# Optimization experiments

Measured on AMD Instinct MI355X. Metric: run time of the kernel, lower is better.

The kernel has to match this reference:

```python
import jax, jax.numpy as jnp
import numpy as np

N_ATOMS = 200000
N_BONDS = 300000
E = 600000
D = 128
H = 128
EPS = 1e-5  # BatchNorm1d default eps


def setup_inputs() -> dict:
    key = jax.random.key(0)
    ks = jax.random.split(key, 8)
    x_atoms = jax.random.normal(ks[0], (N_ATOMS, D), jnp.float32)
    x_bonds = jax.random.normal(ks[1], (N_BONDS, D), jnp.float32)
    # atoms -> bonds edges: row0 src atom idx, row1 dst bond idx
    ei_ab = jnp.stack([
        jax.random.randint(ks[2], (E,), 0, N_ATOMS),
        jax.random.randint(ks[3], (E,), 0, N_BONDS),
    ]).astype(jnp.int64)
    # bonds -> atoms edges
    ei_ba = jnp.stack([
        jax.random.randint(ks[4], (E,), 0, N_BONDS),
        jax.random.randint(ks[5], (E,), 0, N_ATOMS),
    ]).astype(jnp.int64)
    xav = float(np.sqrt(6.0 / (D + H)))
    W = jax.random.uniform(ks[6], (H, D), jnp.float32, -xav, xav)   # shared lin_rel
    b = jnp.zeros((H,), jnp.float32)
    Wr = jax.random.uniform(ks[7], (H, D), jnp.float32, -xav, xav)  # res_connection
    br = jnp.zeros((H,), jnp.float32)
    return {
        "x_atoms": x_atoms, "x_bonds": x_bonds,
        "ei_ab": ei_ab, "ei_ba": ei_ba,
        "W": W, "b": b, "Wr": Wr, "br": br,
        "gamma_atoms": jnp.ones((H,), jnp.float32),
        "beta_atoms": jnp.zeros((H,), jnp.float32),
        "gamma_bonds": jnp.ones((H,), jnp.float32),
        "beta_bonds": jnp.zeros((H,), jnp.float32),
    }


def _bn(v, g, bt):
    # BatchNorm1d training-mode math: batch mean, biased variance
    m = v.mean(axis=0)
    var = v.var(axis=0)
    return (v - m) * jax.lax.rsqrt(var + EPS) * g + bt


def reference(x_atoms, x_bonds, ei_ab, ei_ba, W, b, Wr, br,
              gamma_atoms, beta_atoms, gamma_bonds, beta_bonds):
    # shared lin_rel applied to both node types
    h_atoms = x_atoms @ W.T + b   # [N_ATOMS, H]
    h_bonds = x_bonds @ W.T + b   # [N_BONDS, H]

    # message = lin(x_src)[src], aggregate = scatter-add at dst (source_to_target)
    agg_bonds = jax.ops.segment_sum(h_atoms[ei_ab[0]], ei_ab[1], num_segments=N_BONDS)
    agg_atoms = jax.ops.segment_sum(h_bonds[ei_ba[0]], ei_ba[1], num_segments=N_ATOMS)

    # residual: activation(res_connection(x))
    out_atoms = agg_atoms + jax.nn.relu(x_atoms @ Wr.T + br)
    out_bonds = agg_bonds + jax.nn.relu(x_bonds @ Wr.T + br)

    # dropout is identity in eval/deterministic reference
    out_atoms = _bn(out_atoms, gamma_atoms, beta_atoms)
    out_bonds = _bn(out_bonds, gamma_bonds, beta_bonds)
    return out_atoms, out_bonds
```

## Files before the change

kernel.cpp:

```cpp
#include <hip/hip_runtime.h>
#include <stdint.h>

#define NATOMS 200000
#define NBONDS 300000
#define NEDGE  600000
#define NSEG   (NATOMS + NBONDS)
#define DF     128
#define EPS    1e-5f
#define SCHUNK 2048
#define NSBLK  ((NSEG + SCHUNK - 1) / SCHUNK)
#define NGRP   (NSEG / 16)
#define NBUCK  32
#define NCHA   (NATOMS / 64)
#define NCHB   ((NBONDS + 63) / 64)
#define NCH    (NCHA + NCHB)

typedef __attribute__((ext_vector_type(8))) short bf16x8;
typedef __attribute__((ext_vector_type(4))) float f32x4;
typedef unsigned short u16;

__device__ __forceinline__ short f2b(float f) {
  union { float f; uint32_t u; } v; v.f = f;
  uint32_t r = v.u + 0x7fffu + ((v.u >> 16) & 1u);
  return (short)(r >> 16);
}
__device__ __forceinline__ float bf2f(u16 h) {
  union { uint32_t u; float f; } v; v.u = ((uint32_t)h) << 16; return v.f;
}
__device__ __forceinline__ bf16x8 pack8(float4 u, float4 v) {
  bf16x8 t;
  t[0] = f2b(u.x); t[1] = f2b(u.y); t[2] = f2b(u.z); t[3] = f2b(u.w);
  t[4] = f2b(v.x); t[5] = f2b(v.y); t[6] = f2b(v.z); t[7] = f2b(v.w);
  return t;
}

__global__ void k_prep(const float* __restrict__ W, const float* __restrict__ Wr,
                       u16* __restrict__ Wb, u16* __restrict__ Wrb) {
  int i = blockIdx.x * blockDim.x + threadIdx.x;
  if (i < DF * DF) {
    Wb[i]  = (u16)f2b(W[i]);
    Wrb[i] = (u16)f2b(Wr[i]);
  }
}

__global__ void k_setup(const float* __restrict__ xa, const float* __restrict__ xb,
                        u16* __restrict__ xaT, u16* __restrict__ xbT,
                        const int* __restrict__ ab, const int* __restrict__ ba,
                        int* __restrict__ cnt) {
  const int NA8 = NATOMS * DF / 8;
  const int NT8 = NSEG * DF / 8;
  int bid = blockIdx.x;
  if (bid < 4096) {
    int stride = 4096 * 256;
    for (int i = bid * 256 + threadIdx.x; i < NT8; i += stride) {
      const float* src; u16* dst; int j;
      if (i < NA8) { src = xa; dst = xaT; j = i; }
      else { src = xb; dst = xbT; j = i - NA8; }
      const float4 a = *(const float4*)(src + (size_t)j * 8);
      const float4 b = *(const float4*)(src + (size_t)j * 8 + 4);
      *(bf16x8*)(dst + (size_t)j * 8) = pack8(a, b);
    }
  } else {
    int stride = 512 * 256;
    for (int e = (bid - 4096) * 256 + threadIdx.x; e < 2 * NEDGE; e += stride) {
      int g;
      if (e < NEDGE) g = NATOMS + ab[NEDGE + e];
      else           g = ba[NEDGE + (e - NEDGE)];
      atomicAdd(cnt + g, 1);
    }
  }
}

__global__ void k_hist(const int* __restrict__ ab, const int* __restrict__ ba,
                       int* __restrict__ cnt) {
  int stride = gridDim.x * blockDim.x;
  for (int e = blockIdx.x * blockDim.x + threadIdx.x; e < 2 * NEDGE; e += stride) {
    int g;
    if (e < NEDGE) g = NATOMS + ab[NEDGE + e];
    else           g = ba[NEDGE + (e - NEDGE)];
    atomicAdd(cnt + g, 1);
  }
}

__global__ void k_scanA(const int* __restrict__ cnt, int* __restrict__ bsum) {
  __shared__ int wsm[4];
  int t = threadIdx.x;
  int base = blockIdx.x * SCHUNK + t * 8;
  int s = 0;
#pragma unroll
  for (int j = 0; j < 8; ++j) { int i = base + j; if (i < NSEG) s += cnt[i]; }
  for (int d = 1; d < 64; d <<= 1) s += __shfl_xor(s, d);
  if ((t & 63) == 0) wsm[t >> 6] = s;
  __syncthreads();
  if (t == 0) bsum[blockIdx.x] = wsm[0] + wsm[1] + wsm[2] + wsm[3];
}

__global__ void k_scanB(const int* __restrict__ bsum, int* __restrict__ bbase) {
  __shared__ int wsm[4];
  int t = threadIdx.x;
  int lane = t & 63;
  int v = (t < NSBLK) ? bsum[t] : 0;
  int s = v;
  for (int d = 1; d < 64; d <<= 1) { int n = __shfl_up(s, d); if (lane >= d) s += n; }
  if (lane == 63) wsm[t >> 6] = s;
  __syncthreads();
  int wbase = 0;
  for (int w = 0; w < (t >> 6); ++w) wbase += wsm[w];
  if (t < NSBLK) bbase[t] = wbase + s - v;
}

__global__ void k_scanC(const int* __restrict__ cnt, const int* __restrict__ bbase,
                        int* __restrict__ off, int* __restrict__ cursor) {
  __shared__ int wsm[4];
  int t = threadIdx.x;
  int lane = t & 63, wv = t >> 6;
  int base = blockIdx.x * SCHUNK + t * 8;
  int v[8]; int ts = 0;
#pragma unroll
  for (int j = 0; j < 8; ++j) { int i = base + j; v[j] = (i < NSEG) ? cnt[i] : 0; ts += v[j]; }
  int s = ts;
  for (int d = 1; d < 64; d <<= 1) { int n = __shfl_up(s, d); if (lane >= d) s += n; }
  if (lane == 63) wsm[wv] = s;
  __syncthreads();
  int wbase = bbase[blockIdx.x];
  for (int w = 0; w < wv; ++w) wbase += wsm[w];
  int run = wbase + s - ts;
#pragma unroll
  for (int j = 0; j < 8; ++j) {
    int i = base + j;
    if (i < NSEG) { off[i] = run; cursor[i] = run; }
    run += v[j];
  }
}

__global__ void k_fill(const int* __restrict__ ab, const int* __restrict__ ba,
                       int* __restrict__ cursor, int* __restrict__ sorted) {
  int stride = gridDim.x * blockDim.x;
  for (int e = blockIdx.x * blockDim.x + threadIdx.x; e < 2 * NEDGE; e += stride) {
    int g, src;
    if (e < NEDGE) { g = NATOMS + ab[NEDGE + e]; src = ab[e]; }
    else { int e2 = e - NEDGE; g = ba[NEDGE + e2]; src = ba[e2]; }
    int pos = atomicAdd(cursor + g, 1);
    sorted[pos] = src;
  }
}

__global__ void k_gather_b(const u16* __restrict__ xaT, const u16* __restrict__ xbT,
                           const int* __restrict__ sorted, const int* __restrict__ off,
                           const int* __restrict__ cnt, u16* __restrict__ aggT) {
  int lane = threadIdx.x & 63;
  int l16 = lane & 15, e4 = lane >> 4;
  int wid = (blockIdx.x * blockDim.x + threadIdx.x) >> 6;
  int nw = (gridDim.x * blockDim.x) >> 6;
  for (int g = wid; g < NSEG; g += nw) {
    int start = off[g], deg = cnt[g];
    const u16* src = (g < NATOMS) ? xbT : xaT;
    float acc[8];
#pragma unroll
    for (int j = 0; j < 8; ++j) acc[j] = 0.f;
    for (int k = e4; k < deg; k += 4) {
      int s = sorted[start + k];
      bf16x8 v = *(const bf16x8*)(src + (size_t)s * DF + l16 * 8);
#pragma unroll
      for (int j = 0; j < 8; ++j) acc[j] += bf2f((u16)v[j]);
    }
#pragma unroll
    for (int j = 0; j < 8; ++j) {
      acc[j] += __shfl_xor(acc[j], 16);
      acc[j] += __shfl_xor(acc[j], 32);
    }
    if (e4 == 0) {
      bf16x8 r;
#pragma unroll
      for (int j = 0; j < 8; ++j) r[j] = f2b(acc[j]);
      *(bf16x8*)(aggT + (size_t)g * DF + l16 * 8) = r;
    }
  }
}

__global__ void k_gather_f(const float* __restrict__ xa, const float* __restrict__ xb,
                           const int* __restrict__ sorted, const int* __restrict__ off,
                           const int* __restrict__ cnt, float* __restrict__ outf) {
  int l32 = threadIdx.x & 31;
  int hwid = (blockIdx.x * blockDim.x + threadIdx.x) >> 5;
  int nhw = (gridDim.x * blockDim.x) >> 5;
  for (int g = hwid; g < NSEG; g += nhw) {
    int start = off[g], deg = cnt[g];
    const float* src = (g < NATOMS) ? xb : xa;
    float a0 = 0.f, a1 = 0.f, a2 = 0.f, a3 = 0.f;
    int k = 0;
    for (; k + 1 < deg; k += 2) {
      int s0 = sorted[start + k], s1 = sorted[start + k + 1];
      float4 v0 = *(const float4*)(src + (size_t)s0 * DF + l32 * 4);
      float4 v1 = *(const float4*)(src + (size_t)s1 * DF + l32 * 4);
      a0 += v0.x + v1.x; a1 += v0.y + v1.y; a2 += v0.z + v1.z; a3 += v0.w + v1.w;
    }
    if (k < deg) {
      int s0 = sorted[start + k];
      float4 v0 = *(const float4*)(src + (size_t)s0 * DF + l32 * 4);
      a0 += v0.x; a1 += v0.y; a2 += v0.z; a3 += v0.w;
    }
    float4 r; r.x = a0; r.y = a1; r.z = a2; r.w = a3;
    *(float4*)(outf + (size_t)g * DF + l32 * 4) = r;
  }
}


#define LOADG(G, S) { \
  int sb_ = (G) << 4; \
  int typ_ = sb_ >= NATOMS; \
  const u16* ap_ = aggT + ((size_t)(sb_ + r16) << 7) + kq8; \
  const u16* xp_; \
  if (typ_) xp_ = xbT + ((size_t)(sb_ - NATOMS + r16) << 7) + kq8; \
  else      xp_ = xaT + ((size_t)(sb_ + r16) << 7) + kq8; \
  S##A0 = *(const bf16x8*)(ap_);      S##A1 = *(const bf16x8*)(ap_ + 32); \
  S##A2 = *(const bf16x8*)(ap_ + 64); S##A3 = *(const bf16x8*)(ap_ + 96); \
  S##X0 = *(const bf16x8*)(xp_);      S##X1 = *(const bf16x8*)(xp_ + 32); \
  S##X2 = *(const bf16x8*)(xp_ + 64); S##X3 = *(const bf16x8*)(xp_ + 96); \
  S##C0 = cnt[sb_ + kq4 + 0]; S##C1 = cnt[sb_ + kq4 + 1]; \
  S##C2 = cnt[sb_ + kq4 + 2]; S##C3 = cnt[sb_ + kq4 + 3]; \
}

#define COMPUTE(G, S) { \
  int sb_ = (G) << 4; \
  int typ_ = sb_ >= NATOMS; \
  f32x4 w0 = {0.f,0.f,0.f,0.f}, w1 = {0.f,0.f,0.f,0.f}; \
  f32x4 r0 = {0.f,0.f,0.f,0.f}, r1 = {0.f,0.f,0.f,0.f}; \
  w0 = __builtin_amdgcn_mfma_f32_16x16x32_bf16(S##A0, wf[0][0], w0, 0,0,0); \
  w1 = __builtin_amdgcn_mfma_f32_16x16x32_bf16(S##A0, wf[1][0], w1, 0,0,0); \
  r0 = __builtin_amdgcn_mfma_f32_16x16x32_bf16(S##X0, wrf[0][0], r0, 0,0,0); \
  r1 = __builtin_amdgcn_mfma_f32_16x16x32_bf16(S##X0, wrf[1][0], r1, 0,0,0); \
  w0 = __builtin_amdgcn_mfma_f32_16x16x32_bf16(S##A1, wf[0][1], w0, 0,0,0); \
  w1 = __builtin_amdgcn_mfma_f32_16x16x32_bf16(S##A1, wf[1][1], w1, 0,0,0); \
  r0 = __builtin_amdgcn_mfma_f32_16x16x32_bf16(S##X1, wrf[0][1], r0, 0,0,0); \
  r1 = __builtin_amdgcn_mfma_f32_16x16x32_bf16(S##X1, wrf[1][1], r1, 0,0,0); \
  w0 = __builtin_amdgcn_mfma_f32_16x16x32_bf16(S##A2, wf[0][2], w0, 0,0,0); \
  w1 = __builtin_amdgcn_mfma_f32_16x16x32_bf16(S##A2, wf[1][2], w1, 0,0,0); \
  r0 = __builtin_amdgcn_mfma_f32_16x16x32_bf16(S##X2, wrf[0][2], r0, 0,0,0); \
  r1 = __builtin_amdgcn_mfma_f32_16x16x32_bf16(S##X2, wrf[1][2], r1, 0,0,0); \
  w0 = __builtin_amdgcn_mfma_f32_16x16x32_bf16(S##A3, wf[0][3], w0, 0,0,0); \
  w1 = __builtin_amdgcn_mfma_f32_16x16x32_bf16(S##A3, wf[1][3], w1, 0,0,0); \
  r0 = __builtin_amdgcn_mfma_f32_16x16x32_bf16(S##X3, wrf[0][3], r0, 0,0,0); \
  r1 = __builtin_amdgcn_mfma_f32_16x16x32_bf16(S##X3, wrf[1][3], r1, 0,0,0); \
  const float cf0_ = (float)S##C0, cf1_ = (float)S##C1; \
  const float cf2_ = (float)S##C2, cf3_ = (float)S##C3; \
  u16* gp_ = gT + ((size_t)(sb_ + kq4) << 7) + t016 + r16; \
  float g0_, g1_, g2_, g3_, ss_, qq_; \
  g0_ = w0[0] + cf0_ * bvv0 + fmaxf(r0[0] + brr0, 0.f); \
  g1_ = w0[1] + cf1_ * bvv0 + fmaxf(r0[1] + brr0, 0.f); \
  g2_ = w0[2] + cf2_ * bvv0 + fmaxf(r0[2] + brr0, 0.f); \
  g3_ = w0[3] + cf3_ * bvv0 + fmaxf(r0[3] + brr0, 0.f); \
  gp_[0] = (u16)f2b(g0_); gp_[128] = (u16)f2b(g1_); \
  gp_[256] = (u16)f2b(g2_); gp_[384] = (u16)f2b(g3_); \
  ss_ = g0_ + g1_ + g2_ + g3_; \
  qq_ = g0_*g0_ + g1_*g1_ + g2_*g2_ + g3_*g3_; \
  if (typ_) { sB0 += ss_; qB0 += qq_; } else { sA0 += ss_; qA0 += qq_; } \
  g0_ = w1[0] + cf0_ * bvv1 + fmaxf(r1[0] + brr1, 0.f); \
  g1_ = w1[1] + cf1_ * bvv1 + fmaxf(r1[1] + brr1, 0.f); \
  g2_ = w1[2] + cf2_ * bvv1 + fmaxf(r1[2] + brr1, 0.f); \
  g3_ = w1[3] + cf3_ * bvv1 + fmaxf(r1[3] + brr1, 0.f); \
  gp_[16] = (u16)f2b(g0_); gp_[144] = (u16)f2b(g1_); \
  gp_[272] = (u16)f2b(g2_); gp_[400] = (u16)f2b(g3_); \
  ss_ = g0_ + g1_ + g2_ + g3_; \
  qq_ = g0_*g0_ + g1_*g1_ + g2_*g2_ + g3_*g3_; \
  if (typ_) { sB1 += ss_; qB1 += qq_; } else { sA1 += ss_; qA1 += qq_; } \
}

__global__ __launch_bounds__(256, 2) void k_gemm_p(
    const u16* __restrict__ xaT, const u16* __restrict__ xbT,
    const u16* __restrict__ aggT, u16* __restrict__ gT,
    const int* __restrict__ cnt,
    const u16* __restrict__ Wb, const u16* __restrict__ Wrb,
    const float* __restrict__ bb, const float* __restrict__ brb,
    float* __restrict__ stats) {
  int lane = threadIdx.x & 63;
  int wv = threadIdx.x >> 6;
  int r16 = lane & 15, kq = lane >> 4;
  int kq8 = kq * 8, kq4 = kq * 4;
  int t016 = wv * 32;

  bf16x8 wf[2][4], wrf[2][4];
#pragma unroll
  for (int ti = 0; ti < 2; ++ti) {
#pragma unroll
    for (int kk = 0; kk < 4; ++kk) {
      size_t o = (size_t)(t016 + ti * 16 + r16) * DF + kk * 32 + kq8;
      wf[ti][kk]  = *(const bf16x8*)(Wb + o);
      wrf[ti][kk] = *(const bf16x8*)(Wrb + o);
    }
  }
  float bvv0 = bb[t016 + r16],      brr0 = brb[t016 + r16];
  float bvv1 = bb[t016 + 16 + r16], brr1 = brb[t016 + 16 + r16];

  float sA0 = 0.f, sA1 = 0.f, qA0 = 0.f, qA1 = 0.f;
  float sB0 = 0.f, sB1 = 0.f, qB0 = 0.f, qB1 = 0.f;

  bf16x8 PA0, PA1, PA2, PA3, PX0, PX1, PX2, PX3;
  bf16x8 QA0, QA1, QA2, QA3, QX0, QX1, QX2, QX3;
  int PC0, PC1, PC2, PC3, QC0, QC1, QC2, QC3;

  int step = gridDim.x;
  int g = blockIdx.x;
  if (g < NGRP) { LOADG(g, P); }
  while (g < NGRP) {
    int gn = g + step;
    if (gn < NGRP) { LOADG(gn, Q); }
    COMPUTE(g, P);
    g = gn;
    if (g >= NGRP) break;
    gn = g + step;
    if (gn < NGRP) { LOADG(gn, P); }
    COMPUTE(g, Q);
    g = gn;
  }

  int bkt = blockIdx.x & (NBUCK - 1);
  float* p = stats + (size_t)bkt * 4 * DF;
  {
    float s0 = sA0, q0 = qA0, s1 = sB0, q1 = qB0;
    s0 += __shfl_xor(s0, 16); q0 += __shfl_xor(q0, 16);
    s1 += __shfl_xor(s1, 16); q1 += __shfl_xor(q1, 16);
    s0 += __shfl_xor(s0, 32); q0 += __shfl_xor(q0, 32);
    s1 += __shfl_xor(s1, 32); q1 += __shfl_xor(q1, 32);
    if (kq == 0) {
      int feat = t016 + r16;
      atomicAdd(p + 0 * DF + feat, s0);
      atomicAdd(p + 1 * DF + feat, q0);
      atomicAdd(p + 2 * DF + feat, s1);
      atomicAdd(p + 3 * DF + feat, q1);
    }
  }
  {
    float s0 = sA1, q0 = qA1, s1 = sB1, q1 = qB1;
    s0 += __shfl_xor(s0, 16); q0 += __shfl_xor(q0, 16);
    s1 += __shfl_xor(s1, 16); q1 += __shfl_xor(q1, 16);
    s0 += __shfl_xor(s0, 32); q0 += __shfl_xor(q0, 32);
    s1 += __shfl_xor(s1, 32); q1 += __shfl_xor(q1, 32);
    if (kq == 0) {
      int feat = t016 + 16 + r16;
      atomicAdd(p + 0 * DF + feat, s0);
      atomicAdd(p + 1 * DF + feat, q0);
      atomicAdd(p + 2 * DF + feat, s1);
      atomicAdd(p + 3 * DF + feat, q1);
    }
  }
}

__global__ __launch_bounds__(256, 2) void k_gemm0(
    const float* __restrict__ xa, const float* __restrict__ xb,
    float* __restrict__ outf, const int* __restrict__ cnt,
    const u16* __restrict__ Wb, const u16* __restrict__ Wrb,
    const float* __restrict__ bb, const float* __restrict__ brb,
    float* __restrict__ stats) {
  int lane = threadIdx.x & 63;
  int wv = threadIdx.x >> 6;
  int r16 = lane & 15, kq = lane >> 4;
  int t016 = wv * 32;

  bf16x8 wf[2][4], wrf[2][4];
#pragma unroll
  for (int ti = 0; ti < 2; ++ti) {
#pragma unroll
    for (int kk = 0; kk < 4; ++kk) {
      size_t o = (size_t)(t016 + ti * 16 + r16) * DF + kk * 32 + kq * 8;
      wf[ti][kk]  = *(const bf16x8*)(Wb + o);
      wrf[ti][kk] = *(const bf16x8*)(Wrb + o);
    }
  }
  float bvv[2] = { bb[t016 + r16], bb[t016 + 16 + r16] };
  float brr[2] = { brb[t016 + r16], brb[t016 + 16 + r16] };

  float sA[2] = {0.f, 0.f}, qA[2] = {0.f, 0.f};
  float sB[2] = {0.f, 0.f}, qB[2] = {0.f, 0.f};

  for (int c = blockIdx.x; c < NCH; c += gridDim.x) {
    int typ, nrows, goff, base;
    if (c < NCHA) { typ = 0; nrows = NATOMS; goff = 0; base = c * 64; }
    else { typ = 1; nrows = NBONDS; goff = NATOMS; base = (c - NCHA) * 64; }
    const float* xsrc = typ ? xb : xa;

#pragma unroll
    for (int rg = 0; rg < 4; ++rg) {
      int rowbase = base + rg * 16;
      if (rowbase < nrows) {
        int row = rowbase + r16;
        const float* ap = outf + (size_t)(goff + row) * DF + kq * 8;
        const float* xp = xsrc + (size_t)row * DF + kq * 8;
        bf16x8 fA[4], fX[4];
#pragma unroll
        for (int kk = 0; kk < 4; ++kk) {
          fA[kk] = pack8(*(const float4*)(ap + kk * 32), *(const float4*)(ap + kk * 32 + 4));
          fX[kk] = pack8(*(const float4*)(xp + kk * 32), *(const float4*)(xp + kk * 32 + 4));
        }
        __syncthreads();

        f32x4 accW[2], accR[2];
#pragma unroll
        for (int ti = 0; ti < 2; ++ti) {
#pragma unroll
          for (int r = 0; r < 4; ++r) { accW[ti][r] = 0.f; accR[ti][r] = 0.f; }
        }
#pragma unroll
        for (int kk = 0; kk < 4; ++kk) {
#pragma unroll
          for (int ti = 0; ti < 2; ++ti) {
            accW[ti] = __builtin_amdgcn_mfma_f32_16x16x32_bf16(fA[kk], wf[ti][kk], accW[ti], 0, 0, 0);
            accR[ti] = __builtin_amdgcn_mfma_f32_16x16x32_bf16(fX[kk], wrf[ti][kk], accR[ti], 0, 0, 0);
          }
        }
        float cf[4];
#pragma unroll
        for (int r = 0; r < 4; ++r)
          cf[r] = (float)cnt[goff + rowbase + kq * 4 + r];
#pragma unroll
        for (int ti = 0; ti < 2; ++ti) {
          int feat = t016 + ti * 16 + r16;
          float s = 0.f, q = 0.f;
#pragma unroll
          for (int r = 0; r < 4; ++r) {
            int grow = rowbase + kq * 4 + r;
            float gg = accW[ti][r] + cf[r] * bvv[ti] + fmaxf(accR[ti][r] + brr[ti], 0.f);
            outf[(size_t)(goff + grow) * DF + feat] = gg;
            s += gg; q += gg * gg;
          }
          if (typ == 0) { sA[ti] += s; qA[ti] += q; }
          else          { sB[ti] += s; qB[ti] += q; }
        }
      }
    }
  }

  int bkt = blockIdx.x & (NBUCK - 1);
  float* p = stats + (size_t)bkt * 4 * DF;
#pragma unroll
  for (int ti = 0; ti < 2; ++ti) {
    float s0 = sA[ti], q0 = qA[ti], s1 = sB[ti], q1 = qB[ti];
    s0 += __shfl_xor(s0, 16); q0 += __shfl_xor(q0, 16);
    s1 += __shfl_xor(s1, 16); q1 += __shfl_xor(q1, 16);
    s0 += __shfl_xor(s0, 32); q0 += __shfl_xor(q0, 32);
    s1 += __shfl_xor(s1, 32); q1 += __shfl_xor(q1, 32);
    if (kq == 0) {
      int feat = t016 + ti * 16 + r16;
      atomicAdd(p + 0 * DF + feat, s0);
      atomicAdd(p + 1 * DF + feat, q0);
      atomicAdd(p + 2 * DF + feat, s1);
      atomicAdd(p + 3 * DF + feat, q1);
    }
  }
}

__global__ void k_stats(const float* __restrict__ stats,
                        const float* __restrict__ ga, const float* __restrict__ bea,
                        const float* __restrict__ gb, const float* __restrict__ beb,
                        float* __restrict__ scale, float* __restrict__ shift) {
  int tid = threadIdx.x;
  if (tid < 2 * DF) {
    int t = tid >> 7, f = tid & (DF - 1);
    float S = 0.f, SS = 0.f;
    for (int bk = 0; bk < NBUCK; ++bk) {
      const float* p = stats + (size_t)bk * 4 * DF;
      S  += p[(2 * t) * DF + f];
      SS += p[(2 * t + 1) * DF + f];
    }
    float n = t ? (float)NBONDS : (float)NATOMS;
    float mean = S / n;
    float var = SS / n - mean * mean;
    float rstd = rsqrtf(var + EPS);
    float g = t ? gb[f] : ga[f];
    float be = t ? beb[f] : bea[f];
    scale[tid] = rstd * g;
    shift[tid] = be - mean * rstd * g;
  }
}

template<int TIER>
__global__ void k_norm(float* __restrict__ out, const u16* __restrict__ gT,
                       const float* __restrict__ scale, const float* __restrict__ shift) {
  if constexpr (TIER) {
    const size_t nv = (size_t)NSEG * DF / 8;
    size_t stride = (size_t)gridDim.x * blockDim.x;
    for (size_t i = (size_t)blockIdx.x * blockDim.x + threadIdx.x; i < nv; i += stride) {
      size_t e = i * 8;
      int t = e >= (size_t)NATOMS * DF;
      int f = (int)(e & (DF - 1));
      bf16x8 v = *(const bf16x8*)(gT + e);
      const float* sc = scale + t * DF + f;
      const float* sh = shift + t * DF + f;
      float4 o0, o1;
      o0.x = fmaf(bf2f((u16)v[0]), sc[0], sh[0]);
      o0.y = fmaf(bf2f((u16)v[1]), sc[1], sh[1]);
      o0.z = fmaf(bf2f((u16)v[2]), sc[2], sh[2]);
      o0.w = fmaf(bf2f((u16)v[3]), sc[3], sh[3]);
      o1.x = fmaf(bf2f((u16)v[4]), sc[4], sh[4]);
      o1.y = fmaf(bf2f((u16)v[5]), sc[5], sh[5]);
      o1.z = fmaf(bf2f((u16)v[6]), sc[6], sh[6]);
      o1.w = fmaf(bf2f((u16)v[7]), sc[7], sh[7]);
      *(float4*)(out + e) = o0;
      *(float4*)(out + e + 4) = o1;
    }
  } else {
    const size_t nv = (size_t)NSEG * DF / 4;
    size_t stride = (size_t)gridDim.x * blockDim.x;
    for (size_t i = (size_t)blockIdx.x * blockDim.x + threadIdx.x; i < nv; i += stride) {
      size_t e = i * 4;
      int t = e >= (size_t)NATOMS * DF;
      int f = (int)(e & (DF - 1));
      const float* sc = scale + t * DF + f;
      const float* sh = shift + t * DF + f;
      float4 v = ((float4*)out)[i];
      v.x = fmaf(v.x, sc[0], sh[0]);
      v.y = fmaf(v.y, sc[1], sh[1]);
      v.z = fmaf(v.z, sc[2], sh[2]);
      v.w = fmaf(v.w, sc[3], sh[3]);
      ((float4*)out)[i] = v;
    }
  }
}

extern "C" void kernel_launch(void* const* d_in, const int* in_sizes, int n_in,
                              void* d_out, int out_size, void* d_ws, size_t ws_size,
                              hipStream_t stream) {
  const float* xa  = (const float*)d_in[0];
  const float* xb  = (const float*)d_in[1];
  const int*   ab  = (const int*)d_in[2];
  const int*   ba  = (const int*)d_in[3];
  const float* W   = (const float*)d_in[4];
  const float* b   = (const float*)d_in[5];
  const float* Wr  = (const float*)d_in[6];
  const float* br  = (const float*)d_in[7];
  const float* ga  = (const float*)d_in[8];
  const float* bea = (const float*)d_in[9];
  const float* gb  = (const float*)d_in[10];
  const float* beb = (const float*)d_in[11];
  float* out = (float*)d_out;

  char* ws = (char*)d_ws;
  int*   cnt    = (int*)ws;
  int*   off    = (int*)(ws +  2000000);
  int*   cursor = (int*)(ws +  4000000);
  int*   sorted = (int*)(ws +  6000000);
  float* stats  = (float*)(ws + 10800000);
  int*   bsum   = (int*)(ws + 10865536);
  int*   bbase  = (int*)(ws + 10866560);
  u16*   Wbf    = (u16*)(ws + 10867584);
  u16*   Wrbf   = (u16*)(ws + 10900352);
  float* scale  = (float*)(ws + 10933120);
  float* shift  = (float*)(ws + 10934144);
  u16*   gT   = (u16*)(ws + 10935168);
  u16*   xaT  = (u16*)(ws + 138935168);
  u16*   xbT  = (u16*)(ws + 190135168);
  u16*   aggT = (u16*)(ws + 266935168);
  const bool xt = ws_size >= 394935168ull;

  hipMemsetAsync(cnt, 0, 2000000, stream);
  hipMemsetAsync(stats, 0, 65536, stream);

  k_prep<<<64, 256, 0, stream>>>(W, Wr, Wbf, Wrbf);
  if (xt) {
    k_setup<<<4608, 256, 0, stream>>>(xa, xb, xaT, xbT, ab, ba, cnt);
  } else {
    k_hist<<<2048, 256, 0, stream>>>(ab, ba, cnt);
  }
  k_scanA<<<NSBLK, 256, 0, stream>>>(cnt, bsum);
  k_scanB<<<1, 256, 0, stream>>>(bsum, bbase);
  k_scanC<<<NSBLK, 256, 0, stream>>>(cnt, bbase, off, cursor);
  k_fill<<<2048, 256, 0, stream>>>(ab, ba, cursor, sorted);

  if (xt) {
    k_gather_b<<<8192, 256, 0, stream>>>(xaT, xbT, sorted, off, cnt, aggT);
    k_gemm_p<<<2048, 256, 0, stream>>>(xaT, xbT, aggT, gT, cnt, Wbf, Wrbf, b, br, stats);
    k_stats<<<1, 256, 0, stream>>>(stats, ga, bea, gb, beb, scale, shift);
    k_norm<1><<<4096, 256, 0, stream>>>(out, gT, scale, shift);
  } else {
    k_gather_f<<<8192, 256, 0, stream>>>(xa, xb, sorted, off, cnt, out);
    k_gemm0<<<2048, 256, 0, stream>>>(xa, xb, out, cnt, Wbf, Wrbf, b, br, stats);
    k_stats<<<1, 256, 0, stream>>>(stats, ga, bea, gb, beb, scale, shift);
    k_norm<0><<<8192, 256, 0, stream>>>(out, gT, scale, shift);
  }
}
```

Measured before the change: 630.0 us.

## Fuse gather-aggregate into GEMM kernel via LDS tile, fold weight prep into setup

```diff
diff --git a/kernel.cpp b/kernel.cpp
--- a/kernel.cpp
+++ b/kernel.cpp
@@ -9,7 +9,6 @@
 #define EPS    1e-5f
 #define SCHUNK 2048
 #define NSBLK  ((NSEG + SCHUNK - 1) / SCHUNK)
-#define NGRP   (NSEG / 16)
 #define NBUCK  32
 #define NCHA   (NATOMS / 64)
 #define NCHB   ((NBONDS + 63) / 64)
@@ -46,7 +45,9 @@
 __global__ void k_setup(const float* __restrict__ xa, const float* __restrict__ xb,
                         u16* __restrict__ xaT, u16* __restrict__ xbT,
                         const int* __restrict__ ab, const int* __restrict__ ba,
-                        int* __restrict__ cnt) {
+                        int* __restrict__ cnt,
+                        const float* __restrict__ W, const float* __restrict__ Wr,
+                        u16* __restrict__ Wb, u16* __restrict__ Wrb) {
   const int NA8 = NATOMS * DF / 8;
   const int NT8 = NSEG * DF / 8;
   int bid = blockIdx.x;
@@ -60,13 +61,19 @@
       const float4 b = *(const float4*)(src + (size_t)j * 8 + 4);
       *(bf16x8*)(dst + (size_t)j * 8) = pack8(a, b);
     }
-  } else {
+  } else if (bid < 4608) {
     int stride = 512 * 256;
     for (int e = (bid - 4096) * 256 + threadIdx.x; e < 2 * NEDGE; e += stride) {
       int g;
       if (e < NEDGE) g = NATOMS + ab[NEDGE + e];
       else           g = ba[NEDGE + (e - NEDGE)];
       atomicAdd(cnt + g, 1);
+    }
+  } else {
+    int i = (bid - 4608) * 256 + threadIdx.x;
+    if (i < DF * DF) {
+      Wb[i]  = (u16)f2b(W[i]);
+      Wrb[i] = (u16)f2b(Wr[i]);
     }
   }
 }
@@ -145,35 +152,169 @@
   }
 }
 
-__global__ void k_gather_b(const u16* __restrict__ xaT, const u16* __restrict__ xbT,
-                           const int* __restrict__ sorted, const int* __restrict__ off,
-                           const int* __restrict__ cnt, u16* __restrict__ aggT) {
-  int lane = threadIdx.x & 63;
-  int l16 = lane & 15, e4 = lane >> 4;
-  int wid = (blockIdx.x * blockDim.x + threadIdx.x) >> 6;
-  int nw = (gridDim.x * blockDim.x) >> 6;
-  for (int g = wid; g < NSEG; g += nw) {
-    int start = off[g], deg = cnt[g];
-    const u16* src = (g < NATOMS) ? xbT : xaT;
-    float acc[8];
-#pragma unroll
-    for (int j = 0; j < 8; ++j) acc[j] = 0.f;
-    for (int k = e4; k < deg; k += 4) {
-      int s = sorted[start + k];
-      bf16x8 v = *(const bf16x8*)(src + (size_t)s * DF + l16 * 8);
-#pragma unroll
-      for (int j = 0; j < 8; ++j) acc[j] += bf2f((u16)v[j]);
-    }
-#pragma unroll
-    for (int j = 0; j < 8; ++j) {
-      acc[j] += __shfl_xor(acc[j], 16);
-      acc[j] += __shfl_xor(acc[j], 32);
-    }
-    if (e4 == 0) {
-      bf16x8 r;
-#pragma unroll
-      for (int j = 0; j < 8; ++j) r[j] = f2b(acc[j]);
-      *(bf16x8*)(aggT + (size_t)g * DF + l16 * 8) = r;
+__global__ __launch_bounds__(256, 2) void k_fuse(
+    const u16* __restrict__ xaT, const u16* __restrict__ xbT,
+    const int* __restrict__ sorted, const int* __restrict__ off,
+    const int* __restrict__ cnt, u16* __restrict__ gT,
+    const u16* __restrict__ Wb, const u16* __restrict__ Wrb,
+    const float* __restrict__ bb, const float* __restrict__ brb,
+    float* __restrict__ stats) {
+  __shared__ u16 aggL[64 * DF];
+
+  int tid = threadIdx.x;
+  int lane = tid & 63;
+  int wv = tid >> 6;
+  int r16 = lane & 15, kq = lane >> 4;
+  int t016 = wv * 32;
+  int qw = tid >> 4;
+  int l16 = tid & 15;
+
+  bf16x8 wf[2][4], wrf[2][4];
+#pragma unroll
+  for (int ti = 0; ti < 2; ++ti) {
+#pragma unroll
+    for (int kk = 0; kk < 4; ++kk) {
+      size_t o = (size_t)(t016 + ti * 16 + r16) * DF + kk * 32 + kq * 8;
+      wf[ti][kk]  = *(const bf16x8*)(Wb + o);
+      wrf[ti][kk] = *(const bf16x8*)(Wrb + o);
+    }
+  }
+  float bvv0 = bb[t016 + r16],      brr0 = brb[t016 + r16];
+  float bvv1 = bb[t016 + 16 + r16], brr1 = brb[t016 + 16 + r16];
+
+  float sA0 = 0.f, sA1 = 0.f, qA0 = 0.f, qA1 = 0.f;
+  float sB0 = 0.f, sB1 = 0.f, qB0 = 0.f, qB1 = 0.f;
+
+  for (int c = blockIdx.x; c < NCH; c += gridDim.x) {
+    int typ, nrows, goff, base;
+    if (c < NCHA) { typ = 0; nrows = NATOMS; goff = 0; base = c * 64; }
+    else { typ = 1; nrows = NBONDS; goff = NATOMS; base = (c - NCHA) * 64; }
+    const u16* gsrc = typ ? xaT : xbT;
+    const u16* xsrc = typ ? xbT : xaT;
+
+    __syncthreads();
+
+#pragma unroll
+    for (int i = 0; i < 4; ++i) {
+      int r = qw + i * 16;
+      int row = base + r;
+      if (row < nrows) {
+        int gidx = goff + row;
+        int start = off[gidx], deg = cnt[gidx];
+        float a0 = 0.f, a1 = 0.f, a2 = 0.f, a3 = 0.f;
+        float a4 = 0.f, a5 = 0.f, a6 = 0.f, a7 = 0.f;
+        int k = 0;
+        for (; k + 1 < deg; k += 2) {
+          int s0 = sorted[start + k], s1 = sorted[start + k + 1];
+          bf16x8 v0 = *(const bf16x8*)(gsrc + (size_t)s0 * DF + l16 * 8);
+          bf16x8 v1 = *(const bf16x8*)(gsrc + (size_t)s1 * DF + l16 * 8);
+          a0 += bf2f((u16)v0[0]) + bf2f((u16)v1[0]);
+          a1 += bf2f((u16)v0[1]) + bf2f((u16)v1[1]);
+          a2 += bf2f((u16)v0[2]) + bf2f((u16)v1[2]);
+          a3 += bf2f((u16)v0[3]) + bf2f((u16)v1[3]);
+          a4 += bf2f((u16)v0[4]) + bf2f((u16)v1[4]);
+          a5 += bf2f((u16)v0[5]) + bf2f((u16)v1[5]);
+          a6 += bf2f((u16)v0[6]) + bf2f((u16)v1[6]);
+          a7 += bf2f((u16)v0[7]) + bf2f((u16)v1[7]);
+        }
+        if (k < deg) {
+          int s0 = sorted[start + k];
+          bf16x8 v0 = *(const bf16x8*)(gsrc + (size_t)s0 * DF + l16 * 8);
+          a0 += bf2f((u16)v0[0]); a1 += bf2f((u16)v0[1]);
+          a2 += bf2f((u16)v0[2]); a3 += bf2f((u16)v0[3]);
+          a4 += bf2f((u16)v0[4]); a5 += bf2f((u16)v0[5]);
+          a6 += bf2f((u16)v0[6]); a7 += bf2f((u16)v0[7]);
+        }
+        bf16x8 rr;
+        rr[0] = f2b(a0); rr[1] = f2b(a1); rr[2] = f2b(a2); rr[3] = f2b(a3);
+        rr[4] = f2b(a4); rr[5] = f2b(a5); rr[6] = f2b(a6); rr[7] = f2b(a7);
+        *(bf16x8*)(aggL + r * DF + ((l16 ^ (r & 7)) * 8)) = rr;
+      }
+    }
+    __syncthreads();
+
+#pragma unroll
+    for (int rg = 0; rg < 4; ++rg) {
+      int rowbase = base + rg * 16;
+      if (rowbase < nrows) {
+        int lrow = rg * 16 + r16;
+        bf16x8 fA[4], fX[4];
+#pragma unroll
+        for (int kk = 0; kk < 4; ++kk) {
+          int c8 = (4 * kk + kq) ^ (r16 & 7);
+          fA[kk] = *(const bf16x8*)(aggL + lrow * DF + c8 * 8);
+        }
+        const u16* xp = xsrc + (size_t)(rowbase + r16) * DF + kq * 8;
+#pragma unroll
+        for (int kk = 0; kk < 4; ++kk) fX[kk] = *(const bf16x8*)(xp + kk * 32);
+
+        f32x4 w0 = {0.f,0.f,0.f,0.f}, w1 = {0.f,0.f,0.f,0.f};
+        f32x4 r0 = {0.f,0.f,0.f,0.f}, r1 = {0.f,0.f,0.f,0.f};
+#pragma unroll
+        for (int kk = 0; kk < 4; ++kk) {
+          w0 = __builtin_amdgcn_mfma_f32_16x16x32_bf16(fA[kk], wf[0][kk], w0, 0, 0, 0);
+          w1 = __builtin_amdgcn_mfma_f32_16x16x32_bf16(fA[kk], wf[1][kk], w1, 0, 0, 0);
+          r0 = __builtin_amdgcn_mfma_f32_16x16x32_bf16(fX[kk], wrf[0][kk], r0, 0, 0, 0);
+          r1 = __builtin_amdgcn_mfma_f32_16x16x32_bf16(fX[kk], wrf[1][kk], r1, 0, 0, 0);
+        }
+
+        float cf0 = (float)cnt[goff + rowbase + kq * 4 + 0];
+        float cf1 = (float)cnt[goff + rowbase + kq * 4 + 1];
+        float cf2 = (float)cnt[goff + rowbase + kq * 4 + 2];
+        float cf3 = (float)cnt[goff + rowbase + kq * 4 + 3];
+
+        u16* gp = gT + ((size_t)(goff + rowbase + kq * 4) << 7) + t016 + r16;
+        float g0, g1, g2, g3, ss, qq;
+        g0 = w0[0] + cf0 * bvv0 + fmaxf(r0[0] + brr0, 0.f);
+        g1 = w0[1] + cf1 * bvv0 + fmaxf(r0[1] + brr0, 0.f);
+        g2 = w0[2] + cf2 * bvv0 + fmaxf(r0[2] + brr0, 0.f);
+        g3 = w0[3] + cf3 * bvv0 + fmaxf(r0[3] + brr0, 0.f);
+        gp[0]   = (u16)f2b(g0); gp[128] = (u16)f2b(g1);
+        gp[256] = (u16)f2b(g2); gp[384] = (u16)f2b(g3);
+        ss = g0 + g1 + g2 + g3;
+        qq = g0*g0 + g1*g1 + g2*g2 + g3*g3;
+        if (typ) { sB0 += ss; qB0 += qq; } else { sA0 += ss; qA0 += qq; }
+        g0 = w1[0] + cf0 * bvv1 + fmaxf(r1[0] + brr1, 0.f);
+        g1 = w1[1] + cf1 * bvv1 + fmaxf(r1[1] + brr1, 0.f);
+        g2 = w1[2] + cf2 * bvv1 + fmaxf(r1[2] + brr1, 0.f);
+        g3 = w1[3] + cf3 * bvv1 + fmaxf(r1[3] + brr1, 0.f);
+        gp[16]  = (u16)f2b(g0); gp[144] = (u16)f2b(g1);
+        gp[272] = (u16)f2b(g2); gp[400] = (u16)f2b(g3);
+        ss = g0 + g1 + g2 + g3;
+        qq = g0*g0 + g1*g1 + g2*g2 + g3*g3;
+        if (typ) { sB1 += ss; qB1 += qq; } else { sA1 += ss; qA1 += qq; }
+      }
+    }
+  }
+
+  int bkt = blockIdx.x & (NBUCK - 1);
+  float* p = stats + (size_t)bkt * 4 * DF;
+  {
+    float s0 = sA0, q0 = qA0, s1 = sB0, q1 = qB0;
+    s0 += __shfl_xor(s0, 16); q0 += __shfl_xor(q0, 16);
+    s1 += __shfl_xor(s1, 16); q1 += __shfl_xor(q1, 16);
+    s0 += __shfl_xor(s0, 32); q0 += __shfl_xor(q0, 32);
+    s1 += __shfl_xor(s1, 32); q1 += __shfl_xor(q1, 32);
+    if (kq == 0) {
+      int feat = t016 + r16;
+      atomicAdd(p + 0 * DF + feat, s0);
+      atomicAdd(p + 1 * DF + feat, q0);
+      atomicAdd(p + 2 * DF + feat, s1);
+      atomicAdd(p + 3 * DF + feat, q1);
+    }
+  }
+  {
+    float s0 = sA1, q0 = qA1, s1 = sB1, q1 = qB1;
+    s0 += __shfl_xor(s0, 16); q0 += __shfl_xor(q0, 16);
+    s1 += __shfl_xor(s1, 16); q1 += __shfl_xor(q1, 16);
+    s0 += __shfl_xor(s0, 32); q0 += __shfl_xor(q0, 32);
+    s1 += __shfl_xor(s1, 32); q1 += __shfl_xor(q1, 32);
+    if (kq == 0) {
+      int feat = t016 + 16 + r16;
+      atomicAdd(p + 0 * DF + feat, s0);
+      atomicAdd(p + 1 * DF + feat, q0);
+      atomicAdd(p + 2 * DF + feat, s1);
+      atomicAdd(p + 3 * DF + feat, q1);
     }
   }
 }
@@ -202,147 +343,6 @@
     }
     float4 r; r.x = a0; r.y = a1; r.z = a2; r.w = a3;
     *(float4*)(outf + (size_t)g * DF + l32 * 4) = r;
-  }
-}
-
-
-#define LOADG(G, S) { \
-  int sb_ = (G) << 4; \
-  int typ_ = sb_ >= NATOMS; \
-  const u16* ap_ = aggT + ((size_t)(sb_ + r16) << 7) + kq8; \
-  const u16* xp_; \
-  if (typ_) xp_ = xbT + ((size_t)(sb_ - NATOMS + r16) << 7) + kq8; \
-  else      xp_ = xaT + ((size_t)(sb_ + r16) << 7) + kq8; \
-  S##A0 = *(const bf16x8*)(ap_);      S##A1 = *(const bf16x8*)(ap_ + 32); \
-  S##A2 = *(const bf16x8*)(ap_ + 64); S##A3 = *(const bf16x8*)(ap_ + 96); \
-  S##X0 = *(const bf16x8*)(xp_);      S##X1 = *(const bf16x8*)(xp_ + 32); \
-  S##X2 = *(const bf16x8*)(xp_ + 64); S##X3 = *(const bf16x8*)(xp_ + 96); \
-  S##C0 = cnt[sb_ + kq4 + 0]; S##C1 = cnt[sb_ + kq4 + 1]; \
-  S##C2 = cnt[sb_ + kq4 + 2]; S##C3 = cnt[sb_ + kq4 + 3]; \
-}
-
-#define COMPUTE(G, S) { \
-  int sb_ = (G) << 4; \
-  int typ_ = sb_ >= NATOMS; \
-  f32x4 w0 = {0.f,0.f,0.f,0.f}, w1 = {0.f,0.f,0.f,0.f}; \
-  f32x4 r0 = {0.f,0.f,0.f,0.f}, r1 = {0.f,0.f,0.f,0.f}; \
-  w0 = __builtin_amdgcn_mfma_f32_16x16x32_bf16(S##A0, wf[0][0], w0, 0,0,0); \
-  w1 = __builtin_amdgcn_mfma_f32_16x16x32_bf16(S##A0, wf[1][0], w1, 0,0,0); \
-  r0 = __builtin_amdgcn_mfma_f32_16x16x32_bf16(S##X0, wrf[0][0], r0, 0,0,0); \
-  r1 = __builtin_amdgcn_mfma_f32_16x16x32_bf16(S##X0, wrf[1][0], r1, 0,0,0); \
-  w0 = __builtin_amdgcn_mfma_f32_16x16x32_bf16(S##A1, wf[0][1], w0, 0,0,0); \
-  w1 = __builtin_amdgcn_mfma_f32_16x16x32_bf16(S##A1, wf[1][1], w1, 0,0,0); \
-  r0 = __builtin_amdgcn_mfma_f32_16x16x32_bf16(S##X1, wrf[0][1], r0, 0,0,0); \
-  r1 = __builtin_amdgcn_mfma_f32_16x16x32_bf16(S##X1, wrf[1][1], r1, 0,0,0); \
-  w0 = __builtin_amdgcn_mfma_f32_16x16x32_bf16(S##A2, wf[0][2], w0, 0,0,0); \
-  w1 = __builtin_amdgcn_mfma_f32_16x16x32_bf16(S##A2, wf[1][2], w1, 0,0,0); \
-  r0 = __builtin_amdgcn_mfma_f32_16x16x32_bf16(S##X2, wrf[0][2], r0, 0,0,0); \
-  r1 = __builtin_amdgcn_mfma_f32_16x16x32_bf16(S##X2, wrf[1][2], r1, 0,0,0); \
-  w0 = __builtin_amdgcn_mfma_f32_16x16x32_bf16(S##A3, wf[0][3], w0, 0,0,0); \
-  w1 = __builtin_amdgcn_mfma_f32_16x16x32_bf16(S##A3, wf[1][3], w1, 0,0,0); \
-  r0 = __builtin_amdgcn_mfma_f32_16x16x32_bf16(S##X3, wrf[0][3], r0, 0,0,0); \
-  r1 = __builtin_amdgcn_mfma_f32_16x16x32_bf16(S##X3, wrf[1][3], r1, 0,0,0); \
-  const float cf0_ = (float)S##C0, cf1_ = (float)S##C1; \
-  const float cf2_ = (float)S##C2, cf3_ = (float)S##C3; \
-  u16* gp_ = gT + ((size_t)(sb_ + kq4) << 7) + t016 + r16; \
-  float g0_, g1_, g2_, g3_, ss_, qq_; \
-  g0_ = w0[0] + cf0_ * bvv0 + fmaxf(r0[0] + brr0, 0.f); \
-  g1_ = w0[1] + cf1_ * bvv0 + fmaxf(r0[1] + brr0, 0.f); \
-  g2_ = w0[2] + cf2_ * bvv0 + fmaxf(r0[2] + brr0, 0.f); \
-  g3_ = w0[3] + cf3_ * bvv0 + fmaxf(r0[3] + brr0, 0.f); \
-  gp_[0] = (u16)f2b(g0_); gp_[128] = (u16)f2b(g1_); \
-  gp_[256] = (u16)f2b(g2_); gp_[384] = (u16)f2b(g3_); \
-  ss_ = g0_ + g1_ + g2_ + g3_; \
-  qq_ = g0_*g0_ + g1_*g1_ + g2_*g2_ + g3_*g3_; \
-  if (typ_) { sB0 += ss_; qB0 += qq_; } else { sA0 += ss_; qA0 += qq_; } \
-  g0_ = w1[0] + cf0_ * bvv1 + fmaxf(r1[0] + brr1, 0.f); \
-  g1_ = w1[1] + cf1_ * bvv1 + fmaxf(r1[1] + brr1, 0.f); \
-  g2_ = w1[2] + cf2_ * bvv1 + fmaxf(r1[2] + brr1, 0.f); \
-  g3_ = w1[3] + cf3_ * bvv1 + fmaxf(r1[3] + brr1, 0.f); \
-  gp_[16] = (u16)f2b(g0_); gp_[144] = (u16)f2b(g1_); \
-  gp_[272] = (u16)f2b(g2_); gp_[400] = (u16)f2b(g3_); \
-  ss_ = g0_ + g1_ + g2_ + g3_; \
-  qq_ = g0_*g0_ + g1_*g1_ + g2_*g2_ + g3_*g3_; \
-  if (typ_) { sB1 += ss_; qB1 += qq_; } else { sA1 += ss_; qA1 += qq_; } \
-}
-
-__global__ __launch_bounds__(256, 2) void k_gemm_p(
-    const u16* __restrict__ xaT, const u16* __restrict__ xbT,
-    const u16* __restrict__ aggT, u16* __restrict__ gT,
-    const int* __restrict__ cnt,
-    const u16* __restrict__ Wb, const u16* __restrict__ Wrb,
-    const float* __restrict__ bb, const float* __restrict__ brb,
-    float* __restrict__ stats) {
-  int lane = threadIdx.x & 63;
-  int wv = threadIdx.x >> 6;
-  int r16 = lane & 15, kq = lane >> 4;
-  int kq8 = kq * 8, kq4 = kq * 4;
-  int t016 = wv * 32;
-
-  bf16x8 wf[2][4], wrf[2][4];
-#pragma unroll
-  for (int ti = 0; ti < 2; ++ti) {
-#pragma unroll
-    for (int kk = 0; kk < 4; ++kk) {
-      size_t o = (size_t)(t016 + ti * 16 + r16) * DF + kk * 32 + kq8;
-      wf[ti][kk]  = *(const bf16x8*)(Wb + o);
-      wrf[ti][kk] = *(const bf16x8*)(Wrb + o);
-    }
-  }
-  float bvv0 = bb[t016 + r16],      brr0 = brb[t016 + r16];
-  float bvv1 = bb[t016 + 16 + r16], brr1 = brb[t016 + 16 + r16];
-
-  float sA0 = 0.f, sA1 = 0.f, qA0 = 0.f, qA1 = 0.f;
-  float sB0 = 0.f, sB1 = 0.f, qB0 = 0.f, qB1 = 0.f;
-
-  bf16x8 PA0, PA1, PA2, PA3, PX0, PX1, PX2, PX3;
-  bf16x8 QA0, QA1, QA2, QA3, QX0, QX1, QX2, QX3;
-  int PC0, PC1, PC2, PC3, QC0, QC1, QC2, QC3;
-
-  int step = gridDim.x;
-  int g = blockIdx.x;
-  if (g < NGRP) { LOADG(g, P); }
-  while (g < NGRP) {
-    int gn = g + step;
-    if (gn < NGRP) { LOADG(gn, Q); }
-    COMPUTE(g, P);
-    g = gn;
-    if (g >= NGRP) break;
-    gn = g + step;
-    if (gn < NGRP) { LOADG(gn, P); }
-    COMPUTE(g, Q);
-    g = gn;
-  }
-
-  int bkt = blockIdx.x & (NBUCK - 1);
-  float* p = stats + (size_t)bkt * 4 * DF;
-  {
-    float s0 = sA0, q0 = qA0, s1 = sB0, q1 = qB0;
-    s0 += __shfl_xor(s0, 16); q0 += __shfl_xor(q0, 16);
-    s1 += __shfl_xor(s1, 16); q1 += __shfl_xor(q1, 16);
-    s0 += __shfl_xor(s0, 32); q0 += __shfl_xor(q0, 32);
-    s1 += __shfl_xor(s1, 32); q1 += __shfl_xor(q1, 32);
-    if (kq == 0) {
-      int feat = t016 + r16;
-      atomicAdd(p + 0 * DF + feat, s0);
-      atomicAdd(p + 1 * DF + feat, q0);
-      atomicAdd(p + 2 * DF + feat, s1);
-      atomicAdd(p + 3 * DF + feat, q1);
-    }
-  }
-  {
-    float s0 = sA1, q0 = qA1, s1 = sB1, q1 = qB1;
-    s0 += __shfl_xor(s0, 16); q0 += __shfl_xor(q0, 16);
-    s1 += __shfl_xor(s1, 16); q1 += __shfl_xor(q1, 16);
-    s0 += __shfl_xor(s0, 32); q0 += __shfl_xor(q0, 32);
-    s1 += __shfl_xor(s1, 32); q1 += __shfl_xor(q1, 32);
-    if (kq == 0) {
-      int feat = t016 + 16 + r16;
-      atomicAdd(p + 0 * DF + feat, s0);
-      atomicAdd(p + 1 * DF + feat, q0);
-      atomicAdd(p + 2 * DF + feat, s1);
-      atomicAdd(p + 3 * DF + feat, q1);
-    }
   }
 }
 
@@ -549,16 +549,15 @@
   u16*   gT   = (u16*)(ws + 10935168);
   u16*   xaT  = (u16*)(ws + 138935168);
   u16*   xbT  = (u16*)(ws + 190135168);
-  u16*   aggT = (u16*)(ws + 266935168);
-  const bool xt = ws_size >= 394935168ull;
+  const bool xt = ws_size >= 266935168ull;
 
   hipMemsetAsync(cnt, 0, 2000000, stream);
   hipMemsetAsync(stats, 0, 65536, stream);
 
-  k_prep<<<64, 256, 0, stream>>>(W, Wr, Wbf, Wrbf);
   if (xt) {
-    k_setup<<<4608, 256, 0, stream>>>(xa, xb, xaT, xbT, ab, ba, cnt);
+    k_setup<<<4672, 256, 0, stream>>>(xa, xb, xaT, xbT, ab, ba, cnt, W, Wr, Wbf, Wrbf);
   } else {
+    k_prep<<<64, 256, 0, stream>>>(W, Wr, Wbf, Wrbf);
     k_hist<<<2048, 256, 0, stream>>>(ab, ba, cnt);
   }
   k_scanA<<<NSBLK, 256, 0, stream>>>(cnt, bsum);
@@ -567,8 +566,8 @@
   k_fill<<<2048, 256, 0, stream>>>(ab, ba, cursor, sorted);
 
   if (xt) {
-    k_gather_b<<<8192, 256, 0, stream>>>(xaT, xbT, sorted, off, cnt, aggT);
-    k_gemm_p<<<2048, 256, 0, stream>>>(xaT, xbT, aggT, gT, cnt, Wbf, Wrbf, b, br, stats);
+    k_fuse<<<2048, 256, 0, stream>>>(xaT, xbT, sorted, off, cnt, gT,
+                                     Wbf, Wrbf, b, br, stats);
     k_stats<<<1, 256, 0, stream>>>(stats, ga, bea, gb, beb, scale, shift);
     k_norm<1><<<4096, 256, 0, stream>>>(out, gT, scale, shift);
   } else {
```

Result: faster. 550.7 us (-12.6%).
